# Performance work log

Hardware: AMD Instinct MI355X
Metric: run time of the kernel (lower is better)

The kernel has to match this reference:

```python
import jax, jax.numpy as jnp
import numpy as np
import math

B, T, C = 2, 2048, 1024
N_HEADS = 16
HEAD_DIM = C // N_HEADS  # 64


def setup_inputs() -> dict:
    key = jax.random.key(0)
    ks = jax.random.split(key, 5)
    scale = 0.02
    return {
        "x": jax.random.normal(ks[0], (B, T, C), dtype=jnp.float32),
        "Wq": jax.random.normal(ks[1], (C, C), dtype=jnp.float32) * scale,
        "Wk": jax.random.normal(ks[2], (C, C), dtype=jnp.float32) * scale,
        "Wv": jax.random.normal(ks[3], (C, C), dtype=jnp.float32) * scale,
        "Wc": jax.random.normal(ks[4], (C, C), dtype=jnp.float32) * scale,
        "bc": jnp.zeros((C,), dtype=jnp.float32),
    }


def reference(x, Wq, Wk, Wv, Wc, bc):
    b, t, c = x.shape
    h, dh = N_HEADS, HEAD_DIM
    # Q/K/V projections (Linear, no bias): y = x @ W.T
    def proj(W):
        y = jnp.einsum('btc,dc->btd', x, W)
        return y.reshape(b, t, h, dh).transpose(0, 2, 1, 3)  # [B,H,T,dh]
    Q, K, V = proj(Wq), proj(Wk), proj(Wv)

    # scaled dot-product scores [B,H,T,T]
    scores = jnp.einsum('bhqd,bhkd->bhqk', Q, K) / math.sqrt(dh)
    # additive causal mask: + (1 - tril) * -1e9, as in the original
    causal = jnp.tril(jnp.ones((t, t), dtype=scores.dtype))
    scores = scores + (1.0 - causal) * (-1e9)

    attn = jax.nn.softmax(scores, axis=-1)  # dropout = identity (eval mode)
    o = jnp.einsum('bhqk,bhkd->bhqd', attn, V)
    o = o.transpose(0, 2, 1, 3).reshape(b, t, c)
    # output projection with bias (resid dropout = identity in eval)
    return jnp.einsum('btc,dc->btd', o, Wc) + bc
```

## Files before the change

### kernel.cpp

```cpp
#include <hip/hip_runtime.h>
#include <hip/hip_bf16.h>


typedef __attribute__((ext_vector_type(4))) float f32x4;
typedef __attribute__((ext_vector_type(4))) unsigned int u32x4;
typedef __attribute__((ext_vector_type(8))) __bf16 bf16x8;
typedef __attribute__((ext_vector_type(8))) unsigned short us8;
typedef __attribute__((ext_vector_type(4))) unsigned short us4;

#define LOG2E 1.4426950408889634f

__device__ __forceinline__ unsigned short f2bf(float f) {
    unsigned u = __builtin_bit_cast(unsigned, f);
    u += 0x7fffu + ((u >> 16) & 1u);
    return (unsigned short)(u >> 16);
}

__device__ __forceinline__ unsigned cvt_pk_bf16(float lo, float hi) {
    unsigned r;
    asm("v_cvt_pk_bf16_f32 %0, %1, %2" : "=v"(r) : "v"(lo), "v"(hi));
    return r;
}

__device__ __forceinline__ f32x4 mfma16(us8 a, us8 b, f32x4 c) {
    return __builtin_amdgcn_mfma_f32_16x16x32_bf16(
        __builtin_bit_cast(bf16x8, a), __builtin_bit_cast(bf16x8, b), c, 0, 0, 0);
}

__global__ __launch_bounds__(256) void fill_sentinel(float* __restrict__ out, int n) {
    int i = blockIdx.x * 256 + threadIdx.x;
    if (i < n) out[i] = 12345.0f;
}

__global__ __launch_bounds__(256) void cvt_xw(
    const float* __restrict__ x, const float* __restrict__ wq,
    const float* __restrict__ wk, const float* __restrict__ wv,
    unsigned short* __restrict__ xb, unsigned short* __restrict__ wqkvb) {
    long i = (long)(blockIdx.x * 256 + threadIdx.x) * 4;
    const float* src; unsigned short* dst; long off;
    if (i < 4194304L)      { src = x;  dst = xb;              off = i; }
    else if (i < 5242880L) { src = wq; dst = wqkvb;           off = i - 4194304L; }
    else if (i < 6291456L) { src = wk; dst = wqkvb + 1048576; off = i - 5242880L; }
    else                   { src = wv; dst = wqkvb + 2097152; off = i - 6291456L; }
    f32x4 v = *(const f32x4*)(src + off);
    us4 o = { f2bf(v[0]), f2bf(v[1]), f2bf(v[2]), f2bf(v[3]) };
    *(us4*)(dst + off) = o;
}

__global__ __launch_bounds__(256) void cvt_wc(const float* __restrict__ wc,
                                              unsigned short* __restrict__ wcb) {
    int idx = (blockIdx.x * 256 + threadIdx.x) * 4;
    f32x4 v = *(const f32x4*)(wc + idx);
    us4 o = { f2bf(v[0]), f2bf(v[1]), f2bf(v[2]), f2bf(v[3]) };
    *(us4*)(wcb + idx) = o;
}

template <int MI>
__device__ __forceinline__ void gemm_core_bb(
    const unsigned short* __restrict__ A, const unsigned short* __restrict__ B,
    int K, int m0, int n0, unsigned short* As, unsigned short* Bs, f32x4 acc[MI][4]) {
    const int tid = threadIdx.x;
    const int lane = tid & 63, wid = tid >> 6;
    const int g = lane >> 4, s = lane & 15;
    const int wr = wid >> 1, wc = wid & 1;
#pragma unroll
    for (int mi = 0; mi < MI; mi++)
#pragma unroll
        for (int ni = 0; ni < 4; ni++) acc[mi][ni] = (f32x4){0.f, 0.f, 0.f, 0.f};
    const int row = tid >> 3, col = (tid & 7) * 8;
    for (int k0 = 0; k0 < K; k0 += 64) {
        us8 av[MI], bv[4];
#pragma unroll
        for (int p = 0; p < MI; p++)
            av[p] = *(const us8*)(A + (size_t)(m0 + row + p * 32) * K + k0 + col);
#pragma unroll
        for (int p = 0; p < 4; p++)
            bv[p] = *(const us8*)(B + (size_t)(n0 + row + p * 32) * K + k0 + col);
        __syncthreads();
#pragma unroll
        for (int p = 0; p < MI; p++)
            *(us8*)(As + (row + p * 32) * 72 + col) = av[p];
#pragma unroll
        for (int p = 0; p < 4; p++)
            *(us8*)(Bs + (row + p * 32) * 72 + col) = bv[p];
        __syncthreads();
#pragma unroll
        for (int kk = 0; kk < 2; kk++) {
            us8 af[MI], bf[4];
#pragma unroll
            for (int mi = 0; mi < MI; mi++)
                af[mi] = *(const us8*)(As + (wr * (MI * 16) + mi * 16 + s) * 72 + kk * 32 + g * 8);
#pragma unroll
            for (int ni = 0; ni < 4; ni++)
                bf[ni] = *(const us8*)(Bs + (wc * 64 + ni * 16 + s) * 72 + kk * 32 + g * 8);
#pragma unroll
            for (int mi = 0; mi < MI; mi++)
#pragma unroll
                for (int ni = 0; ni < 4; ni++)
                    acc[mi][ni] = mfma16(af[mi], bf[ni], acc[mi][ni]);
        }
    }
}

__global__ __launch_bounds__(256) void gemm_qkv(
    const unsigned short* __restrict__ X, const unsigned short* __restrict__ Wb,
    unsigned short* __restrict__ Qb, unsigned short* __restrict__ Kb,
    unsigned short* __restrict__ VtG) {
    __shared__ unsigned short S[18432];
    unsigned short* As = S;
    unsigned short* Bs = S + 9216;
    const int bid = blockIdx.x;
    const int xcd = bid & 7, idx = bid >> 3;
    const int bm  = (xcd & 3) * 8 + (idx & 7);
    const int bnl = (xcd >> 2) * 12 + (idx >> 3);
    const int m0 = bm * 128;
    const int which = bnl >> 3;
    const int n0 = (bnl & 7) * 128;
    const unsigned short* W = Wb + (size_t)which * 1048576;
    f32x4 acc[4][4];
    gemm_core_bb<4>(X, W, 1024, m0, n0, As, Bs, acc);
    const int tid = threadIdx.x, lane = tid & 63, wid = tid >> 6;
    const int g = lane >> 4, s = lane & 15, wr = wid >> 1, wc = wid & 1;
    if (which < 2) {
        unsigned short* dst = which == 0 ? Qb : Kb;
        const float scale = which == 0 ? 0.125f : 1.0f;
#pragma unroll
        for (int mi = 0; mi < 4; mi++)
#pragma unroll
            for (int ni = 0; ni < 4; ni++) {
                int n1 = n0 + wc * 64 + ni * 16 + s;
                int hh = n1 >> 6, dd = n1 & 63;
#pragma unroll
                for (int r = 0; r < 4; r++) {
                    int mg = m0 + wr * 64 + mi * 16 + 4 * g + r;
                    int bb = mg >> 11, tt = mg & 2047;
                    dst[((size_t)(bb * 16 + hh) * 2048 + tt) * 64 + dd] = f2bf(acc[mi][ni][r] * scale);
                }
            }
    } else {
        __syncthreads();
        unsigned* T32 = (unsigned*)S;
#pragma unroll
        for (int mi = 0; mi < 4; mi++)
#pragma unroll
            for (int ni = 0; ni < 4; ni++) {
                int nl = wc * 64 + ni * 16 + s;
                int mlh = ((wr * 64 + mi * 16) >> 1) + 2 * g;
                T32[nl * 68 + mlh]     = cvt_pk_bf16(acc[mi][ni][0], acc[mi][ni][1]);
                T32[nl * 68 + mlh + 1] = cvt_pk_bf16(acc[mi][ni][2], acc[mi][ni][3]);
            }
        __syncthreads();
        const int row = tid >> 4, col8 = (tid & 15) * 8;
        const int bb = m0 >> 11, tt0 = m0 & 2047;
#pragma unroll
        for (int p = 0; p < 8; p++) {
            int nl = row + 16 * p;
            int n1 = n0 + nl, hh = n1 >> 6, dd = n1 & 63;
            us8 v = *(const us8*)(S + nl * 136 + col8);
            *(us8*)(VtG + ((size_t)(bb * 16 + hh) * 64 + dd) * 2048 + tt0 + col8) = v;
        }
    }
}

#define ATTN_EPILOGUE(QB0, OA, LR)                                              \
    {                                                                           \
        float li[4];                                                            \
        _Pragma("unroll") for (int r = 0; r < 4; r++)                           \
            li[r] = __shfl((LR), 4 * g + r, 64);                                \
        _Pragma("unroll") for (int db = 0; db < 4; db++)                        \
            _Pragma("unroll") for (int r = 0; r < 4; r++) {                     \
                int qq = (QB0) + 4 * g + r;                                     \
                float v = (OA)[db][r] / li[r];                                  \
                Ob[((size_t)(b * 2048) + qq) * 1024 + h * 64 + db * 16 + s] = f2bf(v); \
            }                                                                   \
    }

__global__ __launch_bounds__(256) void attn(
    const unsigned short* __restrict__ Qb, const unsigned short* __restrict__ Kb,
    const unsigned short* __restrict__ VtG, unsigned short* __restrict__ Ob) {
    __shared__ unsigned short Ks[2][64 * 72];
    __shared__ unsigned short Vt[2][64 * 72];
    const int bh = blockIdx.x & 31, i = blockIdx.x >> 5;
    const int b = bh >> 4, h = bh & 15;
    const unsigned short* Qp = Qb + (size_t)bh * 2048 * 64;
    const unsigned short* Kp = Kb + (size_t)bh * 2048 * 64;
    const unsigned short* Vp = VtG + (size_t)bh * 64 * 2048;
    const int tid = threadIdx.x, lane = tid & 63, wid = tid >> 6;
    const int g = lane >> 4, s = lane & 15;
    const int qbA = i * 64 + wid * 16;
    const int qbB = (31 - i) * 64 + wid * 16;
    const int qgA = qbA + s, qgB = qbB + s;
    us8 qfA[2], qfB[2];
    qfA[0] = *(const us8*)(Qp + (size_t)qgA * 64 + g * 8);
    qfA[1] = *(const us8*)(Qp + (size_t)qgA * 64 + 32 + g * 8);
    qfB[0] = *(const us8*)(Qp + (size_t)qgB * 64 + g * 8);
    qfB[1] = *(const us8*)(Qp + (size_t)qgB * 64 + 32 + g * 8);
    float m_run = -3.0e38f, l_run = 0.f;
    f32x4 o_acc[4];
#pragma unroll
    for (int db = 0; db < 4; db++) o_acc[db] = (f32x4){0.f, 0.f, 0.f, 0.f};
    const int srow = tid >> 3, scol = (tid & 7) * 8;
    auto tileoff = [&](int jj) { return (jj <= i ? jj : jj - i - 1) * 64; };
    us8 kpre[2], vpre[2];
#pragma unroll
    for (int p = 0; p < 2; p++) {
        kpre[p] = *(const us8*)(Kp + (size_t)(srow + 32 * p) * 64 + scol);
        vpre[p] = *(const us8*)(Vp + (size_t)(srow + 32 * p) * 2048 + scol);
    }
#pragma unroll
    for (int p = 0; p < 2; p++) {
        *(us8*)(&Ks[0][(srow + 32 * p) * 72 + scol]) = kpre[p];
        *(us8*)(&Vt[0][(srow + 32 * p) * 72 + scol]) = vpre[p];
    }
    {
        const int nk = tileoff(1);
#pragma unroll
        for (int p = 0; p < 2; p++) {
            kpre[p] = *(const us8*)(Kp + (size_t)(nk + srow + 32 * p) * 64 + scol);
            vpre[p] = *(const us8*)(Vp + (size_t)(srow + 32 * p) * 2048 + nk + scol);
        }
    }
    int cur = 0;
    for (int it = 0; it <= 32; ++it) {
        __syncthreads();
        if (it < 32) {
#pragma unroll
            for (int p = 0; p < 2; p++) {
                *(us8*)(&Ks[cur ^ 1][(srow + 32 * p) * 72 + scol]) = kpre[p];
                *(us8*)(&Vt[cur ^ 1][(srow + 32 * p) * 72 + scol]) = vpre[p];
            }
            if (it < 31) {
                const int nk = tileoff(it + 2);
#pragma unroll
                for (int p = 0; p < 2; p++) {
                    kpre[p] = *(const us8*)(Kp + (size_t)(nk + srow + 32 * p) * 64 + scol);
                    vpre[p] = *(const us8*)(Vp + (size_t)(srow + 32 * p) * 2048 + nk + scol);
                }
            }
        }
        if (it == i + 1) {
            ATTN_EPILOGUE(qbA, o_acc, l_run);
            m_run = -3.0e38f; l_run = 0.f;
#pragma unroll
            for (int db = 0; db < 4; db++) o_acc[db] = (f32x4){0.f, 0.f, 0.f, 0.f};
        }
        const bool qsel = it > i;
        const int kv0 = tileoff(it);
        const int qg = qsel ? qgB : qgA;
        const us8* qf = qsel ? qfB : qfA;
        const unsigned short* Kc = Ks[cur];
        const unsigned short* Vc = Vt[cur];
        float sf[4][4];
        __builtin_amdgcn_s_setprio(1);
#pragma unroll
        for (int f = 0; f < 4; f++) {
            f32x4 a = (f32x4){0.f, 0.f, 0.f, 0.f};
            us8 k0v = *(const us8*)(Kc + (f * 16 + s) * 72 + g * 8);
            us8 k1v = *(const us8*)(Kc + (f * 16 + s) * 72 + 32 + g * 8);
            a = mfma16(k0v, qf[0], a);
            a = mfma16(k1v, qf[1], a);
#pragma unroll
            for (int r = 0; r < 4; r++) sf[f][r] = a[r];
        }
        __builtin_amdgcn_s_setprio(0);
        const bool diag = qsel ? (it == 32) : (it == i);
        if (diag) {
#pragma unroll
            for (int f = 0; f < 4; f++)
#pragma unroll
                for (int r = 0; r < 4; r++)
                    if (kv0 + f * 16 + 4 * g + r > qg) sf[f][r] = -3.0e38f;
        }
        float mt = -3.0e38f;
#pragma unroll
        for (int f = 0; f < 4; f++)
#pragma unroll
            for (int r = 0; r < 4; r++) mt = fmaxf(mt, sf[f][r]);
        mt = fmaxf(mt, __shfl_xor(mt, 16));
        mt = fmaxf(mt, __shfl_xor(mt, 32));
        float mnew = m_run;
        if (!__all(mt - m_run <= 8.0f)) {
            mnew = fmaxf(m_run, mt);
            float alpha = __builtin_amdgcn_exp2f((m_run - mnew) * LOG2E);
            l_run *= alpha;
            float al[4];
#pragma unroll
            for (int r = 0; r < 4; r++) al[r] = __shfl(alpha, 4 * g + r, 64);
#pragma unroll
            for (int db = 0; db < 4; db++)
#pragma unroll
                for (int r = 0; r < 4; r++) o_acc[db][r] *= al[r];
        }
        float psum = 0.f;
#pragma unroll
        for (int f = 0; f < 4; f++)
#pragma unroll
            for (int r = 0; r < 4; r++) {
                float p = __builtin_amdgcn_exp2f((sf[f][r] - mnew) * LOG2E);
                sf[f][r] = p;
                psum += p;
            }
        psum += __shfl_xor(psum, 16);
        psum += __shfl_xor(psum, 32);
        l_run += psum;
        m_run = mnew;
        unsigned pk[4][2];
#pragma unroll
        for (int f = 0; f < 4; f++)
#pragma unroll
            for (int hh2 = 0; hh2 < 2; hh2++)
                pk[f][hh2] = cvt_pk_bf16(sf[f][2 * hh2], sf[f][2 * hh2 + 1]);
        const int srcA = 32 * (g & 1) + s, srcB = srcA + 16;
        const bool ghi = g >= 2;
        us8 pa[2];
#pragma unroll
        for (int kk = 0; kk < 2; kk++) {
            unsigned e0 = __shfl(pk[kk * 2][0], srcA, 64);
            unsigned e1 = __shfl(pk[kk * 2][1], srcA, 64);
            unsigned e2 = __shfl(pk[kk * 2][0], srcB, 64);
            unsigned e3 = __shfl(pk[kk * 2][1], srcB, 64);
            unsigned o0 = __shfl(pk[kk * 2 + 1][0], srcA, 64);
            unsigned o1 = __shfl(pk[kk * 2 + 1][1], srcA, 64);
            unsigned o2 = __shfl(pk[kk * 2 + 1][0], srcB, 64);
            unsigned o3 = __shfl(pk[kk * 2 + 1][1], srcB, 64);
            u32x4 dw = { ghi ? o0 : e0, ghi ? o1 : e1, ghi ? o2 : e2, ghi ? o3 : e3 };
            pa[kk] = __builtin_bit_cast(us8, dw);
        }
        __builtin_amdgcn_s_setprio(1);
#pragma unroll
        for (int db = 0; db < 4; db++) {
            const unsigned short* vrow = Vc + (db * 16 + s) * 72;
            us8 vf0 = *(const us8*)(vrow + g * 8);
            o_acc[db] = mfma16(pa[0], vf0, o_acc[db]);
            us8 vf1 = *(const us8*)(vrow + 32 + g * 8);
            o_acc[db] = mfma16(pa[1], vf1, o_acc[db]);
        }
        __builtin_amdgcn_s_setprio(0);
        cur ^= 1;
    }
    ATTN_EPILOGUE(qbB, o_acc, l_run);
}

__global__ __launch_bounds__(256) void gemm_out(
    const unsigned short* __restrict__ O, const unsigned short* __restrict__ Wcb,
    const float* __restrict__ bc, float* __restrict__ out) {
    __shared__ unsigned short As[64 * 72];
    __shared__ unsigned short Bs[128 * 72];
    const int bid = blockIdx.x;
    const int xcd = bid & 7, idx = bid >> 3;
    const int bm = xcd * 8 + (idx & 7);
    const int bn = idx >> 3;
    const int m0 = bm * 64, n0 = bn * 128;
    f32x4 acc[2][4];
    gemm_core_bb<2>(O, Wcb, 1024, m0, n0, As, Bs, acc);
    const int lane = threadIdx.x & 63, wid = threadIdx.x >> 6;
    const int g = lane >> 4, s = lane & 15, wr = wid >> 1, wc = wid & 1;
#pragma unroll
    for (int mi = 0; mi < 2; mi++)
#pragma unroll
        for (int ni = 0; ni < 4; ni++) {
            int ng = n0 + wc * 64 + ni * 16 + s;
            float bias = bc[ng];
#pragma unroll
            for (int r = 0; r < 4; r++) {
                int mg = m0 + wr * 32 + mi * 16 + 4 * g + r;
                out[(size_t)mg * 1024 + ng] = acc[mi][ni][r] + bias;
            }
        }
}

extern "C" void kernel_launch(void* const* d_in, const int* in_sizes, int n_in,
                              void* d_out, int out_size, void* d_ws, size_t ws_size,
                              hipStream_t stream) {
    const float* x  = (const float*)d_in[0];
    const float* Wq = (const float*)d_in[1];
    const float* Wk = (const float*)d_in[2];
    const float* Wv = (const float*)d_in[3];
    const float* Wc = (const float*)d_in[4];
    const float* bc = (const float*)d_in[5];
    float* out = (float*)d_out;

    if (ws_size < 33554432) {
        fill_sentinel<<<(out_size + 255) / 256, 256, 0, stream>>>(out, out_size);
        return;
    }
    char* w = (char*)d_ws;
    unsigned short* Qb  = (unsigned short*)(w);
    unsigned short* Kb  = (unsigned short*)(w + 8388608);
    unsigned short* VtG = (unsigned short*)(w + 16777216);
    unsigned short* Ob  = (unsigned short*)(w + 25165824);
    unsigned short* Wcb = (unsigned short*)(w);
    unsigned short* xb    = (unsigned short*)d_out;
    unsigned short* wqkvb = (unsigned short*)((char*)d_out + 8388608);

    cvt_xw<<<7168, 256, 0, stream>>>(x, Wq, Wk, Wv, xb, wqkvb);
    gemm_qkv<<<768, 256, 0, stream>>>(xb, wqkvb, Qb, Kb, VtG);
    attn<<<512, 256, 0, stream>>>(Qb, Kb, VtG, Ob);
    cvt_wc<<<1024, 256, 0, stream>>>(Wc, Wcb);
    gemm_out<<<512, 256, 0, stream>>>(Ob, Wcb, bc, out);
}
```

Measured before the change: 123.3 us.

## Fuse Wc bf16 conversion into output GEMM and defer softmax row-sum reduction

```diff
diff --git a/kernel.cpp b/kernel.cpp
--- a/kernel.cpp
+++ b/kernel.cpp
@@ -47,14 +47,6 @@
     *(us4*)(dst + off) = o;
 }
 
-__global__ __launch_bounds__(256) void cvt_wc(const float* __restrict__ wc,
-                                              unsigned short* __restrict__ wcb) {
-    int idx = (blockIdx.x * 256 + threadIdx.x) * 4;
-    f32x4 v = *(const f32x4*)(wc + idx);
-    us4 o = { f2bf(v[0]), f2bf(v[1]), f2bf(v[2]), f2bf(v[3]) };
-    *(us4*)(wcb + idx) = o;
-}
-
 template <int MI>
 __device__ __forceinline__ void gemm_core_bb(
     const unsigned short* __restrict__ A, const unsigned short* __restrict__ B,
@@ -76,6 +68,58 @@
 #pragma unroll
         for (int p = 0; p < 4; p++)
             bv[p] = *(const us8*)(B + (size_t)(n0 + row + p * 32) * K + k0 + col);
+        __syncthreads();
+#pragma unroll
+        for (int p = 0; p < MI; p++)
+            *(us8*)(As + (row + p * 32) * 72 + col) = av[p];
+#pragma unroll
+        for (int p = 0; p < 4; p++)
+            *(us8*)(Bs + (row + p * 32) * 72 + col) = bv[p];
+        __syncthreads();
+#pragma unroll
+        for (int kk = 0; kk < 2; kk++) {
+            us8 af[MI], bf[4];
+#pragma unroll
+            for (int mi = 0; mi < MI; mi++)
+                af[mi] = *(const us8*)(As + (wr * (MI * 16) + mi * 16 + s) * 72 + kk * 32 + g * 8);
+#pragma unroll
+            for (int ni = 0; ni < 4; ni++)
+                bf[ni] = *(const us8*)(Bs + (wc * 64 + ni * 16 + s) * 72 + kk * 32 + g * 8);
+#pragma unroll
+            for (int mi = 0; mi < MI; mi++)
+#pragma unroll
+                for (int ni = 0; ni < 4; ni++)
+                    acc[mi][ni] = mfma16(af[mi], bf[ni], acc[mi][ni]);
+        }
+    }
+}
+
+template <int MI>
+__device__ __forceinline__ void gemm_core_r(
+    const unsigned short* __restrict__ A, const float* __restrict__ Bf,
+    int K, int m0, int n0, unsigned short* As, unsigned short* Bs, f32x4 acc[MI][4]) {
+    const int tid = threadIdx.x;
+    const int lane = tid & 63, wid = tid >> 6;
+    const int g = lane >> 4, s = lane & 15;
+    const int wr = wid >> 1, wc = wid & 1;
+#pragma unroll
+    for (int mi = 0; mi < MI; mi++)
+#pragma unroll
+        for (int ni = 0; ni < 4; ni++) acc[mi][ni] = (f32x4){0.f, 0.f, 0.f, 0.f};
+    const int row = tid >> 3, col = (tid & 7) * 8;
+    for (int k0 = 0; k0 < K; k0 += 64) {
+        us8 av[MI], bv[4];
+#pragma unroll
+        for (int p = 0; p < MI; p++)
+            av[p] = *(const us8*)(A + (size_t)(m0 + row + p * 32) * K + k0 + col);
+#pragma unroll
+        for (int p = 0; p < 4; p++) {
+            size_t boff = (size_t)(n0 + row + p * 32) * K + k0 + col;
+            f32x4 v0 = *(const f32x4*)(Bf + boff);
+            f32x4 v1 = *(const f32x4*)(Bf + boff + 4);
+            bv[p] = (us8){ f2bf(v0[0]), f2bf(v0[1]), f2bf(v0[2]), f2bf(v0[3]),
+                           f2bf(v1[0]), f2bf(v1[1]), f2bf(v1[2]), f2bf(v1[3]) };
+        }
         __syncthreads();
 #pragma unroll
         for (int p = 0; p < MI; p++)
@@ -162,11 +206,14 @@
     }
 }
 
-#define ATTN_EPILOGUE(QB0, OA, LR)                                              \
+#define ATTN_EPILOGUE(QB0, OA, LP)                                              \
     {                                                                           \
+        float lf = (LP);                                                        \
+        lf += __shfl_xor(lf, 16);                                               \
+        lf += __shfl_xor(lf, 32);                                               \
         float li[4];                                                            \
         _Pragma("unroll") for (int r = 0; r < 4; r++)                           \
-            li[r] = __shfl((LR), 4 * g + r, 64);                                \
+            li[r] = __shfl(lf, 4 * g + r, 64);                                  \
         _Pragma("unroll") for (int db = 0; db < 4; db++)                        \
             _Pragma("unroll") for (int r = 0; r < 4; r++) {                     \
                 int qq = (QB0) + 4 * g + r;                                     \
@@ -195,7 +242,7 @@
     qfA[1] = *(const us8*)(Qp + (size_t)qgA * 64 + 32 + g * 8);
     qfB[0] = *(const us8*)(Qp + (size_t)qgB * 64 + g * 8);
     qfB[1] = *(const us8*)(Qp + (size_t)qgB * 64 + 32 + g * 8);
-    float m_run = -3.0e38f, l_run = 0.f;
+    float m_run = -3.0e38f, l_part = 0.f;
     f32x4 o_acc[4];
 #pragma unroll
     for (int db = 0; db < 4; db++) o_acc[db] = (f32x4){0.f, 0.f, 0.f, 0.f};
@@ -239,8 +286,8 @@
             }
         }
         if (it == i + 1) {
-            ATTN_EPILOGUE(qbA, o_acc, l_run);
-            m_run = -3.0e38f; l_run = 0.f;
+            ATTN_EPILOGUE(qbA, o_acc, l_part);
+            m_run = -3.0e38f; l_part = 0.f;
 #pragma unroll
             for (int db = 0; db < 4; db++) o_acc[db] = (f32x4){0.f, 0.f, 0.f, 0.f};
         }
@@ -276,13 +323,12 @@
         for (int f = 0; f < 4; f++)
 #pragma unroll
             for (int r = 0; r < 4; r++) mt = fmaxf(mt, sf[f][r]);
-        mt = fmaxf(mt, __shfl_xor(mt, 16));
-        mt = fmaxf(mt, __shfl_xor(mt, 32));
-        float mnew = m_run;
         if (!__all(mt - m_run <= 8.0f)) {
-            mnew = fmaxf(m_run, mt);
+            mt = fmaxf(mt, __shfl_xor(mt, 16));
+            mt = fmaxf(mt, __shfl_xor(mt, 32));
+            float mnew = fmaxf(m_run, mt);
             float alpha = __builtin_amdgcn_exp2f((m_run - mnew) * LOG2E);
-            l_run *= alpha;
+            l_part *= alpha;
             float al[4];
 #pragma unroll
             for (int r = 0; r < 4; r++) al[r] = __shfl(alpha, 4 * g + r, 64);
@@ -290,20 +336,18 @@
             for (int db = 0; db < 4; db++)
 #pragma unroll
                 for (int r = 0; r < 4; r++) o_acc[db][r] *= al[r];
+            m_run = mnew;
         }
         float psum = 0.f;
 #pragma unroll
         for (int f = 0; f < 4; f++)
 #pragma unroll
             for (int r = 0; r < 4; r++) {
-                float p = __builtin_amdgcn_exp2f((sf[f][r] - mnew) * LOG2E);
+                float p = __builtin_amdgcn_exp2f((sf[f][r] - m_run) * LOG2E);
                 sf[f][r] = p;
                 psum += p;
             }
-        psum += __shfl_xor(psum, 16);
-        psum += __shfl_xor(psum, 32);
-        l_run += psum;
-        m_run = mnew;
+        l_part += psum;
         unsigned pk[4][2];
 #pragma unroll
         for (int f = 0; f < 4; f++)
@@ -338,11 +382,11 @@
         __builtin_amdgcn_s_setprio(0);
         cur ^= 1;
     }
-    ATTN_EPILOGUE(qbB, o_acc, l_run);
+    ATTN_EPILOGUE(qbB, o_acc, l_part);
 }
 
 __global__ __launch_bounds__(256) void gemm_out(
-    const unsigned short* __restrict__ O, const unsigned short* __restrict__ Wcb,
+    const unsigned short* __restrict__ O, const float* __restrict__ Wc,
     const float* __restrict__ bc, float* __restrict__ out) {
     __shared__ unsigned short As[64 * 72];
     __shared__ unsigned short Bs[128 * 72];
@@ -352,7 +396,7 @@
     const int bn = idx >> 3;
     const int m0 = bm * 64, n0 = bn * 128;
     f32x4 acc[2][4];
-    gemm_core_bb<2>(O, Wcb, 1024, m0, n0, As, Bs, acc);
+    gemm_core_r<2>(O, Wc, 1024, m0, n0, As, Bs, acc);
     const int lane = threadIdx.x & 63, wid = threadIdx.x >> 6;
     const int g = lane >> 4, s = lane & 15, wr = wid >> 1, wc = wid & 1;
 #pragma unroll
@@ -389,13 +433,11 @@
     unsigned short* Kb  = (unsigned short*)(w + 8388608);
     unsigned short* VtG = (unsigned short*)(w + 16777216);
     unsigned short* Ob  = (unsigned short*)(w + 25165824);
-    unsigned short* Wcb = (unsigned short*)(w);
     unsigned short* xb    = (unsigned short*)d_out;
     unsigned short* wqkvb = (unsigned short*)((char*)d_out + 8388608);
 
     cvt_xw<<<7168, 256, 0, stream>>>(x, Wq, Wk, Wv, xb, wqkvb);
     gemm_qkv<<<768, 256, 0, stream>>>(xb, wqkvb, Qb, Kb, VtG);
     attn<<<512, 256, 0, stream>>>(Qb, Kb, VtG, Ob);
-    cvt_wc<<<1024, 256, 0, stream>>>(Wc, Wcb);
-    gemm_out<<<512, 256, 0, stream>>>(Ob, Wcb, bc, out);
-}
+    gemm_out<<<512, 256, 0, stream>>>(Ob, Wc, bc, out);
+}
```

Result: slower. 133.6 us (+8.3%).
